# Optimization experiments

Measured on AMD Instinct MI355X. Metric: run time of the kernel, lower is better.

## Reference

```python
import jax, jax.numpy as jnp
import numpy as np


def setup_inputs() -> dict:
    key = jax.random.key(0)
    ks = jax.random.split(key, 7)
    B, C, T = 64, 2048, 256  # T must equal C // heads (see module's matmul(attn, v))
    s = 0.02
    return {
        "x": jax.random.normal(ks[0], (B, C, T), dtype=jnp.float32),
        "Wq": jax.random.normal(ks[1], (C, C), dtype=jnp.float32) * s,
        "bq": jax.random.normal(ks[2], (C,), dtype=jnp.float32) * s,
        "Wk": jax.random.normal(ks[3], (C, C), dtype=jnp.float32) * s,
        "bk": jax.random.normal(ks[4], (C,), dtype=jnp.float32) * s,
        "Wv": jax.random.normal(ks[5], (C, C), dtype=jnp.float32) * s,
        "bv": jax.random.normal(ks[6], (C,), dtype=jnp.float32) * s,
        "heads": 8,
    }


def reference(x, Wq, bq, Wk, bk, Wv, bv, heads):
    B, C, T = x.shape
    H = heads
    D = C // H  # must equal T for this module's math
    scale = float(D) ** -0.5

    def proj(W, b):
        # 1x1 Conv1d == per-timestep linear: out[b,o,t] = sum_c W[o,c] x[b,c,t] + b[o]
        return jnp.einsum('oc,bct->bot', W, x) + b[None, :, None]

    q = proj(Wq, bq).reshape(B, H, D, T).transpose(0, 1, 3, 2)  # (B,H,T,D)
    k = proj(Wk, bk).reshape(B, H, D, T).transpose(0, 1, 3, 2)  # (B,H,T,D)
    v = proj(Wv, bv).reshape(B, H, D, T)                         # (B,H,D,T), D==T

    attn = jax.nn.softmax(jnp.einsum('bhid,bhjd->bhij', q, k) * scale, axis=-1)  # (B,H,T,T)
    # Faithful to torch: matmul(attn, v) with v UNpermuted -> contract attn's last axis with v's D axis
    out = jnp.einsum('bhik,bhkj->bhij', attn, v)  # (B,H,T,T)
    return out.reshape(B, C, T)
```

## Files before the change

### kernel.cpp

```cpp
#include <hip/hip_runtime.h>


typedef __attribute__((ext_vector_type(8))) short    bf16x8;
typedef __attribute__((ext_vector_type(4))) float    f32x4;
typedef __attribute__((ext_vector_type(4))) unsigned short us4;
typedef __attribute__((ext_vector_type(8))) unsigned short us8;
typedef unsigned short u16;
typedef unsigned int   u32;

#define CC 2048
#define TT 256
#define BB 64
#define HH 8
#define DD 256

__device__ __forceinline__ u16 f2bf(float f) {
  u32 u = __builtin_bit_cast(u32, f);
  u32 r = (u + 0x7fffu + ((u >> 16) & 1u)) >> 16;
  return (u16)r;
}
__device__ __forceinline__ float bf2f(u16 b) {
  u32 u = ((u32)b) << 16;
  return __builtin_bit_cast(float, u);
}

__device__ __forceinline__ void async16(const void* g, void* l) {
  __builtin_amdgcn_global_load_lds(
      (const __attribute__((address_space(1))) u32*)g,
      (__attribute__((address_space(3))) u32*)l, 16, 0, 0);
}

__global__ __launch_bounds__(256) void wconv_kernel(
    const float* __restrict__ w0, const float* __restrict__ w1,
    const float* __restrict__ w2, u16* __restrict__ dst) {
  int p = blockIdx.y;
  const float* s = (p == 0) ? w0 : (p == 1) ? w1 : w2;
  size_t i = ((size_t)blockIdx.x * 256 + threadIdx.x) * 4;
  float4 v = *(const float4*)(s + i);
  us4 o = {f2bf(v.x), f2bf(v.y), f2bf(v.z), f2bf(v.w)};
  *(us4*)(dst + (size_t)p * CC * CC + i) = o;
}

__global__ __launch_bounds__(256) void xt_kernel(
    const float* __restrict__ x, u16* __restrict__ xT) {
  __shared__ float tile[64][68];
  int t0 = blockIdx.x * 64;
  int c0 = blockIdx.y * 64;
  int b  = blockIdx.z;
  int tid = threadIdx.x;
  int lr = tid >> 4;
  int lc = (tid & 15) * 4;
  const float* src = x + ((size_t)b * CC + c0) * TT + t0;
#pragma unroll
  for (int s = 0; s < 4; ++s) {
    int c = s * 16 + lr;
    float4 v = *(const float4*)(src + (size_t)c * TT + lc);
    *(float4*)&tile[c][lc] = v;
  }
  __syncthreads();
  int t  = tid >> 2;
  int cb = (tid & 3) * 16;
  u16 tmp[16];
#pragma unroll
  for (int e = 0; e < 16; ++e) tmp[e] = f2bf(tile[cb + e][t]);
  u16* dst = xT + ((size_t)b * TT + t0 + t) * CC + c0 + cb;
  *(us8*)dst       = *(const us8*)&tmp[0];
  *(us8*)(dst + 8) = *(const us8*)&tmp[8];
}

__global__ __launch_bounds__(256) void proj_kernel(
    const u16* __restrict__ Wbf, const u16* __restrict__ xT,
    const float* __restrict__ bq, const float* __restrict__ bk,
    const float* __restrict__ bv, u16* __restrict__ qkv) {
  __shared__ __align__(16) u16 As[128 * 32];
  __shared__ __align__(16) u16 Bs[128 * 32];
  int tid = threadIdx.x;
  int m0 = blockIdx.x * 128;
  int t0 = blockIdx.y * 128;
  int z  = blockIdx.z;
  int proj = z >> 6;
  int b    = z & 63;
  const u16* A = Wbf + (size_t)proj * CC * CC;
  const u16* X = xT + (size_t)b * TT * CC;
  const float* bias = (proj == 0) ? bq : (proj == 1) ? bk : bv;
  u16* outp = qkv + (size_t)proj * BB * CC * TT;

  int lane = tid & 63, w = tid >> 6;
  int wm = w >> 1, wn = w & 1;
  int ar = lane & 15, kq = lane >> 4;

  int arow = tid >> 2;
  int acol = (tid & 3) * 8;
  const u16* Abase = A + (size_t)(m0 + arow) * CC + acol;
  const u16* Xbase = X + (size_t)(t0 + arow) * CC + acol;

  f32x4 acc[4][4] = {};
  for (int k0 = 0; k0 < CC; k0 += 32) {
    async16(Abase + k0, As + tid * 8);
    async16(Abase + (size_t)64 * CC + k0, As + 2048 + tid * 8);
    async16(Xbase + k0, Bs + tid * 8);
    async16(Xbase + (size_t)64 * CC + k0, Bs + 2048 + tid * 8);
    __syncthreads();
    bf16x8 af[4], bfv[4];
#pragma unroll
    for (int mt = 0; mt < 4; ++mt)
      af[mt] = *(const bf16x8*)&As[(wm * 64 + mt * 16 + ar) * 32 + kq * 8];
#pragma unroll
    for (int nt = 0; nt < 4; ++nt)
      bfv[nt] = *(const bf16x8*)&Bs[(wn * 64 + nt * 16 + ar) * 32 + kq * 8];
#pragma unroll
    for (int mt = 0; mt < 4; ++mt)
#pragma unroll
      for (int nt = 0; nt < 4; ++nt)
        acc[mt][nt] = __builtin_amdgcn_mfma_f32_16x16x32_bf16(
            af[mt], bfv[nt], acc[mt][nt], 0, 0, 0);
    __syncthreads();
  }
#pragma unroll
  for (int mt = 0; mt < 4; ++mt) {
    int ob = m0 + wm * 64 + mt * 16 + kq * 4;
    float b0 = bias[ob], b1 = bias[ob + 1], b2 = bias[ob + 2], b3 = bias[ob + 3];
    int h = ob >> 8, d = ob & 255;
    u16* obase = outp + (((size_t)b * HH + h) * TT) * DD + d;
#pragma unroll
    for (int nt = 0; nt < 4; ++nt) {
      int t = t0 + wn * 64 + nt * 16 + ar;
      f32x4 v = acc[mt][nt];
      us4 pk = {f2bf(v[0] + b0), f2bf(v[1] + b1), f2bf(v[2] + b2),
                f2bf(v[3] + b3)};
      *(us4*)(obase + (size_t)t * DD) = pk;
    }
  }
}

__global__ __launch_bounds__(256) void attn_kernel(
    const u16* __restrict__ qkv, float* __restrict__ out) {
  __shared__ __align__(16) u16 As[64 * 32];
  __shared__ __align__(16) u16 Bs[256 * 32];
  __shared__ __align__(16) u16 Ps[64 * 264];
  __shared__ float rowpart[64][4];
  __shared__ float inv[64];

  int tid = threadIdx.x;
  int i0 = blockIdx.x * 64;
  int bh = blockIdx.y;
  const size_t hd = (size_t)TT * DD;
  const u16* Q = qkv + (size_t)bh * hd;
  const u16* K = qkv + (size_t)(BB * HH + bh) * hd;
  const u16* V = qkv + (size_t)(2 * BB * HH + bh) * hd;

  int lane = tid & 63, w = tid >> 6;
  int ar = lane & 15, kq = lane >> 4;
  int arow = tid >> 2, acol = (tid & 3) * 8;

  const u16* Qbase = Q + (size_t)(i0 + arow) * DD + acol;
  const u16* Kbase = K + (size_t)arow * DD + acol;
  const u16* Vbase = V + (size_t)arow * DD + acol;

  f32x4 acc[4][4] = {};
  for (int k0 = 0; k0 < DD; k0 += 32) {
    async16(Qbase + k0, As + tid * 8);
#pragma unroll
    for (int s = 0; s < 4; ++s)
      async16(Kbase + (size_t)(s * 64) * DD + k0, Bs + s * 2048 + tid * 8);
    __syncthreads();
    bf16x8 af[4], bfv[4];
#pragma unroll
    for (int mt = 0; mt < 4; ++mt)
      af[mt] = *(const bf16x8*)&As[(mt * 16 + ar) * 32 + kq * 8];
#pragma unroll
    for (int nt = 0; nt < 4; ++nt)
      bfv[nt] = *(const bf16x8*)&Bs[(w * 64 + nt * 16 + ar) * 32 + kq * 8];
#pragma unroll
    for (int mt = 0; mt < 4; ++mt)
#pragma unroll
      for (int nt = 0; nt < 4; ++nt)
        acc[mt][nt] = __builtin_amdgcn_mfma_f32_16x16x32_bf16(
            af[mt], bfv[nt], acc[mt][nt], 0, 0, 0);
    __syncthreads();
  }
  const float scale = 0.0625f;
#pragma unroll
  for (int mt = 0; mt < 4; ++mt) {
    float ps[4] = {0.f, 0.f, 0.f, 0.f};
#pragma unroll
    for (int nt = 0; nt < 4; ++nt) {
      f32x4 v = acc[mt][nt];
#pragma unroll
      for (int r = 0; r < 4; ++r) {
        float p = __expf(v[r] * scale);
        u16 pb = f2bf(p);
        Ps[(mt * 16 + kq * 4 + r) * 264 + (w * 64 + nt * 16 + ar)] = pb;
        ps[r] += bf2f(pb);
      }
    }
#pragma unroll
    for (int r = 0; r < 4; ++r) {
      float s = ps[r];
      s += __shfl_xor(s, 1, 64);
      s += __shfl_xor(s, 2, 64);
      s += __shfl_xor(s, 4, 64);
      s += __shfl_xor(s, 8, 64);
      if (ar == 0) rowpart[mt * 16 + kq * 4 + r][w] = s;
    }
  }
  __syncthreads();
  if (tid < 64) {
    float s = rowpart[tid][0] + rowpart[tid][1] + rowpart[tid][2] +
              rowpart[tid][3];
    inv[tid] = 1.0f / s;
  }
#pragma unroll
  for (int mt = 0; mt < 4; ++mt)
#pragma unroll
    for (int nt = 0; nt < 4; ++nt) acc[mt][nt] = (f32x4){0.f, 0.f, 0.f, 0.f};
  for (int k0 = 0; k0 < TT; k0 += 32) {
#pragma unroll
    for (int s = 0; s < 4; ++s)
      async16(Vbase + (size_t)(s * 64) * DD + k0, Bs + s * 2048 + tid * 8);
    __syncthreads();
    bf16x8 af[4], bfv[4];
#pragma unroll
    for (int mt = 0; mt < 4; ++mt)
      af[mt] = *(const bf16x8*)&Ps[(mt * 16 + ar) * 264 + k0 + kq * 8];
#pragma unroll
    for (int nt = 0; nt < 4; ++nt)
      bfv[nt] = *(const bf16x8*)&Bs[(w * 64 + nt * 16 + ar) * 32 + kq * 8];
#pragma unroll
    for (int mt = 0; mt < 4; ++mt)
#pragma unroll
      for (int nt = 0; nt < 4; ++nt)
        acc[mt][nt] = __builtin_amdgcn_mfma_f32_16x16x32_bf16(
            af[mt], bfv[nt], acc[mt][nt], 0, 0, 0);
    __syncthreads();
  }
  int b = bh >> 3, h = bh & 7;
  float* obase = out + ((size_t)b * CC + h * TT + i0) * TT;
#pragma unroll
  for (int mt = 0; mt < 4; ++mt)
#pragma unroll
    for (int r = 0; r < 4; ++r) {
      int m = mt * 16 + kq * 4 + r;
      float iv = inv[m];
#pragma unroll
      for (int nt = 0; nt < 4; ++nt) {
        int n = w * 64 + nt * 16 + ar;
        obase[(size_t)m * TT + n] = acc[mt][nt][r] * iv;
      }
    }
}

extern "C" void kernel_launch(void* const* d_in, const int* in_sizes, int n_in,
                              void* d_out, int out_size, void* d_ws,
                              size_t ws_size, hipStream_t stream) {
  const float* x  = (const float*)d_in[0];
  const float* Wq = (const float*)d_in[1];
  const float* bq = (const float*)d_in[2];
  const float* Wk = (const float*)d_in[3];
  const float* bk = (const float*)d_in[4];
  const float* Wv = (const float*)d_in[5];
  const float* bv = (const float*)d_in[6];
  float* out = (float*)d_out;

  char* ws = (char*)d_ws;
  u16* xT  = (u16*)ws;
  u16* Wbf = (u16*)(ws + 67108864);
  u16* qkv = (u16*)(ws + 67108864 + 25165824);

  wconv_kernel<<<dim3(4096, 3, 1), 256, 0, stream>>>(Wq, Wk, Wv, Wbf);
  xt_kernel<<<dim3(4, 32, 64), 256, 0, stream>>>(x, xT);
  proj_kernel<<<dim3(16, 2, 192), 256, 0, stream>>>(Wbf, xT, bq, bk, bv, qkv);
  attn_kernel<<<dim3(4, 512, 1), 256, 0, stream>>>(qkv, out);
}
```

Baseline: 860.1 us.

## Rewrite projection GEMM as 256x256-tile double-buffered pipelined kernel

Replaces the 128x128, single-buffered projection GEMM with a 256x256-tile, 512-thread kernel. It double-buffers LDS over 64-wide K steps and interleaves async global loads with MFMA phases using explicit waitcnt, barriers and setprio. It also XOR-swizzles the LDS layout to cut bank conflicts and remaps block IDs so blocks sharing a weight tile are spread across XCDs. The larger tile raises arithmetic intensity and hides load latency, at the cost of much higher LDS use (128KB per block) and heavier register pressure.

```diff
diff --git a/kernel.cpp b/kernel.cpp
--- a/kernel.cpp
+++ b/kernel.cpp
@@ -68,69 +68,160 @@
   *(us8*)(dst + 8) = *(const us8*)&tmp[8];
 }
 
-__global__ __launch_bounds__(256) void proj_kernel(
+__global__ __launch_bounds__(512, 2) void proj_kernel(
     const u16* __restrict__ Wbf, const u16* __restrict__ xT,
     const float* __restrict__ bq, const float* __restrict__ bk,
     const float* __restrict__ bv, u16* __restrict__ qkv) {
-  __shared__ __align__(16) u16 As[128 * 32];
-  __shared__ __align__(16) u16 Bs[128 * 32];
+  __shared__ __align__(16) u16 As[2][16384];
+  __shared__ __align__(16) u16 Bs[2][16384];
+
   int tid = threadIdx.x;
-  int m0 = blockIdx.x * 128;
-  int t0 = blockIdx.y * 128;
-  int z  = blockIdx.z;
-  int proj = z >> 6;
-  int b    = z & 63;
-  const u16* A = Wbf + (size_t)proj * CC * CC;
-  const u16* X = xT + (size_t)b * TT * CC;
+  int bid = blockIdx.x;
+  int wg  = (bid & 7) * 192 + (bid >> 3);
+  int pm  = wg >> 6;
+  int b   = wg & 63;
+  int proj = pm >> 3;
+  int mt   = pm & 7;
+  int m0   = mt << 8;
+
+  const u16* Ap = Wbf + (size_t)proj * CC * CC + (size_t)m0 * CC;
+  const u16* Xp = xT + (size_t)b * TT * CC;
   const float* bias = (proj == 0) ? bq : (proj == 1) ? bk : bv;
-  u16* outp = qkv + (size_t)proj * BB * CC * TT;
 
   int lane = tid & 63, w = tid >> 6;
-  int wm = w >> 1, wn = w & 1;
+  int wm = w >> 2, wn = w & 3;
   int ar = lane & 15, kq = lane >> 4;
 
-  int arow = tid >> 2;
-  int acol = (tid & 3) * 8;
-  const u16* Abase = A + (size_t)(m0 + arow) * CC + acol;
-  const u16* Xbase = X + (size_t)(t0 + arow) * CC + acol;
-
-  f32x4 acc[4][4] = {};
-  for (int k0 = 0; k0 < CC; k0 += 32) {
-    async16(Abase + k0, As + tid * 8);
-    async16(Abase + (size_t)64 * CC + k0, As + 2048 + tid * 8);
-    async16(Xbase + k0, Bs + tid * 8);
-    async16(Xbase + (size_t)64 * CC + k0, Bs + 2048 + tid * 8);
-    __syncthreads();
-    bf16x8 af[4], bfv[4];
-#pragma unroll
-    for (int mt = 0; mt < 4; ++mt)
-      af[mt] = *(const bf16x8*)&As[(wm * 64 + mt * 16 + ar) * 32 + kq * 8];
-#pragma unroll
-    for (int nt = 0; nt < 4; ++nt)
-      bfv[nt] = *(const bf16x8*)&Bs[(wn * 64 + nt * 16 + ar) * 32 + kq * 8];
-#pragma unroll
-    for (int mt = 0; mt < 4; ++mt)
-#pragma unroll
-      for (int nt = 0; nt < 4; ++nt)
-        acc[mt][nt] = __builtin_amdgcn_mfma_f32_16x16x32_bf16(
-            af[mt], bfv[nt], acc[mt][nt], 0, 0, 0);
-    __syncthreads();
-  }
-#pragma unroll
-  for (int mt = 0; mt < 4; ++mt) {
-    int ob = m0 + wm * 64 + mt * 16 + kq * 4;
-    float b0 = bias[ob], b1 = bias[ob + 1], b2 = bias[ob + 2], b3 = bias[ob + 3];
-    int h = ob >> 8, d = ob & 255;
-    u16* obase = outp + (((size_t)b * HH + h) * TT) * DD + d;
-#pragma unroll
-    for (int nt = 0; nt < 4; ++nt) {
-      int t = t0 + wn * 64 + nt * 16 + ar;
-      f32x4 v = acc[mt][nt];
+  int r_b = tid >> 3;
+  int c8  = tid & 7;
+  int c8s = c8 ^ (((r_b >> 2) & 1) << 1);
+  const size_t go = (size_t)r_b * CC + (size_t)c8s * 8;
+  const int ldsq = r_b * 64 + c8 * 8;
+
+  const int csw  = ((ar >> 2) & 1) << 4;
+  const int col0 = (kq * 8) ^ csw;
+
+  const int arow = wm * 16 + ar;
+  const int brow = wn * 16 + ar;
+
+#define STG_A(buf, kt, h)                                                     \
+  do {                                                                        \
+    async16(Ap + (size_t)((h) * 128) * CC + (size_t)(kt) * 64 + go,           \
+            &As[buf][(h) * 8192 + ldsq]);                                     \
+    async16(Ap + (size_t)((h) * 128 + 64) * CC + (size_t)(kt) * 64 + go,      \
+            &As[buf][(h) * 8192 + 4096 + ldsq]);                              \
+  } while (0)
+#define STG_B(buf, kt, h)                                                     \
+  do {                                                                        \
+    async16(Xp + (size_t)((h) * 128) * CC + (size_t)(kt) * 64 + go,           \
+            &Bs[buf][(h) * 8192 + ldsq]);                                     \
+    async16(Xp + (size_t)((h) * 128 + 64) * CC + (size_t)(kt) * 64 + go,      \
+            &Bs[buf][(h) * 8192 + 4096 + ldsq]);                              \
+  } while (0)
+
+  bf16x8 af[4][2], bfr[2][2];
+  f32x4 acc[8][4] = {};
+
+#define LDA(buf, mh)                                                          \
+  do {                                                                        \
+    _Pragma("unroll") for (int fl = 0; fl < 4; ++fl) {                        \
+      int row = ((mh) * 4 + fl) * 32 + arow;                                  \
+      af[fl][0] = *(const bf16x8*)&As[buf][row * 64 + col0];                  \
+      af[fl][1] = *(const bf16x8*)&As[buf][row * 64 + col0 + 32];             \
+    }                                                                         \
+  } while (0)
+#define LDB(buf, nh)                                                          \
+  do {                                                                        \
+    _Pragma("unroll") for (int gl = 0; gl < 2; ++gl) {                        \
+      int row = ((nh) * 2 + gl) * 64 + brow;                                  \
+      bfr[gl][0] = *(const bf16x8*)&Bs[buf][row * 64 + col0];                 \
+      bfr[gl][1] = *(const bf16x8*)&Bs[buf][row * 64 + col0 + 32];            \
+    }                                                                         \
+  } while (0)
+#define MMA(mh, nh)                                                           \
+  do {                                                                        \
+    _Pragma("unroll") for (int fl = 0; fl < 4; ++fl) {                        \
+      _Pragma("unroll") for (int gl = 0; gl < 2; ++gl) {                      \
+        acc[(mh) * 4 + fl][(nh) * 2 + gl] =                                   \
+            __builtin_amdgcn_mfma_f32_16x16x32_bf16(                          \
+                af[fl][0], bfr[gl][0], acc[(mh) * 4 + fl][(nh) * 2 + gl], 0,  \
+                0, 0);                                                        \
+        acc[(mh) * 4 + fl][(nh) * 2 + gl] =                                   \
+            __builtin_amdgcn_mfma_f32_16x16x32_bf16(                          \
+                af[fl][1], bfr[gl][1], acc[(mh) * 4 + fl][(nh) * 2 + gl], 0,  \
+                0, 0);                                                        \
+      }                                                                       \
+    }                                                                         \
+  } while (0)
+#define PRE(buf, mh, nh)                                                      \
+  do {                                                                        \
+    if ((nh) == 0) LDA(buf, mh);                                              \
+    LDB(buf, nh);                                                             \
+  } while (0)
+#define POST(mh, nh)                                                          \
+  do {                                                                        \
+    __builtin_amdgcn_s_barrier();                                             \
+    asm volatile("s_waitcnt lgkmcnt(0)" ::: "memory");                        \
+    __builtin_amdgcn_sched_barrier(0);                                        \
+    __builtin_amdgcn_s_setprio(1);                                            \
+    MMA(mh, nh);                                                              \
+    __builtin_amdgcn_s_setprio(0);                                            \
+    __builtin_amdgcn_sched_barrier(0);                                        \
+    __builtin_amdgcn_s_barrier();                                             \
+  } while (0)
+#define VM4 asm volatile("s_waitcnt vmcnt(4)" ::: "memory")
+#define VM0 asm volatile("s_waitcnt vmcnt(0)" ::: "memory")
+
+  STG_A(0, 0, 0); STG_B(0, 0, 0); STG_A(0, 0, 1); STG_B(0, 0, 1);
+  STG_A(1, 1, 0); STG_B(1, 1, 0);
+  VM4;
+  __builtin_amdgcn_s_barrier();
+
+  for (int i = 0; i < 15; ++i) {
+    int k = 2 * i;
+    PRE(0, 0, 0); STG_A(1, k + 1, 1);      POST(0, 0);
+    PRE(0, 0, 1); STG_B(1, k + 1, 1);      POST(0, 1);
+    PRE(0, 1, 0); STG_A(0, k + 2, 0);      POST(1, 0);
+    PRE(0, 1, 1); STG_B(0, k + 2, 0); VM4; POST(1, 1);
+    PRE(1, 0, 0); STG_A(0, k + 2, 1);      POST(0, 0);
+    PRE(1, 0, 1); STG_B(0, k + 2, 1);      POST(0, 1);
+    PRE(1, 1, 0); STG_A(1, k + 3, 0);      POST(1, 0);
+    PRE(1, 1, 1); STG_B(1, k + 3, 0); VM4; POST(1, 1);
+  }
+  PRE(0, 0, 0); STG_A(1, 31, 1);           POST(0, 0);
+  PRE(0, 0, 1); STG_B(1, 31, 1);           POST(0, 1);
+  PRE(0, 1, 0);                            POST(1, 0);
+  PRE(0, 1, 1);                       VM0; POST(1, 1);
+  PRE(1, 0, 0);                            POST(0, 0);
+  PRE(1, 0, 1);                            POST(0, 1);
+  PRE(1, 1, 0);                            POST(1, 0);
+  PRE(1, 1, 1);                            POST(1, 1);
+
+  u16* outp = qkv + (size_t)proj * BB * CC * TT +
+              (size_t)(b * HH + mt) * TT * DD;
+#pragma unroll
+  for (int f = 0; f < 8; ++f) {
+    int d0 = f * 32 + wm * 16 + kq * 4;
+    float b0 = bias[m0 + d0],     b1 = bias[m0 + d0 + 1];
+    float b2 = bias[m0 + d0 + 2], b3 = bias[m0 + d0 + 3];
+#pragma unroll
+    for (int g = 0; g < 4; ++g) {
+      int t = g * 64 + wn * 16 + ar;
+      f32x4 v = acc[f][g];
       us4 pk = {f2bf(v[0] + b0), f2bf(v[1] + b1), f2bf(v[2] + b2),
                 f2bf(v[3] + b3)};
-      *(us4*)(obase + (size_t)t * DD) = pk;
+      *(us4*)(outp + (size_t)t * DD + d0) = pk;
     }
   }
+#undef STG_A
+#undef STG_B
+#undef LDA
+#undef LDB
+#undef MMA
+#undef PRE
+#undef POST
+#undef VM4
+#undef VM0
 }
 
 __global__ __launch_bounds__(256) void attn_kernel(
@@ -269,6 +360,6 @@
 
   wconv_kernel<<<dim3(4096, 3, 1), 256, 0, stream>>>(Wq, Wk, Wv, Wbf);
   xt_kernel<<<dim3(4, 32, 64), 256, 0, stream>>>(x, xT);
-  proj_kernel<<<dim3(16, 2, 192), 256, 0, stream>>>(Wbf, xT, bq, bk, bv, qkv);
+  proj_kernel<<<dim3(1536, 1, 1), 512, 0, stream>>>(Wbf, xT, bq, bk, bv, qkv);
   attn_kernel<<<dim3(4, 512, 1), 256, 0, stream>>>(qkv, out);
 }
```

Result: slower. 923.1 us (+7.3%).
